# Kernel optimization log

Hardware: AMD Instinct MI355X
Metric: run time of the kernel (lower is better)

Reference implementation:

```python
import jax, jax.numpy as jnp
import numpy as np

BS, P, MAX_GT, C_IN, NCLS = 16, 4096, 32, 512, 4


def _make_boxes(key, shape):
    k1, k2, k3, k4 = jax.random.split(key, 4)
    x0 = jax.random.uniform(k1, shape) * 500.0
    y0 = jax.random.uniform(k2, shape) * 500.0
    w = 10.0 + jax.random.uniform(k3, shape) * 90.0
    h = 10.0 + jax.random.uniform(k4, shape) * 90.0
    return jnp.stack([x0, y0, x0 + w, y0 + h], -1)


def setup_inputs() -> dict:
    key = jax.random.key(0)
    ks = jax.random.split(key, 10)
    v = jax.random.normal(ks[0], (BS * P, C_IN), jnp.float32)
    rois = _make_boxes(ks[1], (BS, P))
    gt_boxes = _make_boxes(ks[2], (BS, MAX_GT))
    gt_counts = jax.random.randint(ks[3], (BS,), 0, MAX_GT + 1, jnp.int32)
    lab_idx = jax.random.randint(ks[4], (BS,), 0, NCLS)
    labels = jax.nn.one_hot(lab_idx, NCLS, dtype=jnp.float32)
    pre_score = jax.random.uniform(ks[5], (BS, P, NCLS), dtype=jnp.float32)
    cls_w = jax.random.normal(ks[6], (NCLS, C_IN), jnp.float32) * 0.01
    cls_b = jnp.full((NCLS,), -np.log((1.0 - 0.01) / 0.01), jnp.float32)
    reg_w = jax.random.normal(ks[7], (NCLS, C_IN), jnp.float32) * 0.01
    reg_b = jnp.zeros((NCLS,), jnp.float32)
    return {"v": v, "gt_boxes": gt_boxes, "gt_counts": gt_counts, "rois": rois,
            "labels": labels, "pre_score": pre_score, "cls_w": cls_w,
            "cls_b": cls_b, "reg_w": reg_w, "reg_b": reg_b}


def _box_iou(a, b):
    # a: (bs, Na, 4), b: (bs, Nb, 4) -> (bs, Na, Nb)
    area_a = (a[..., 2] - a[..., 0]) * (a[..., 3] - a[..., 1])
    area_b = (b[..., 2] - b[..., 0]) * (b[..., 3] - b[..., 1])
    lt = jnp.maximum(a[..., :, None, :2], b[..., None, :, :2])
    rb = jnp.minimum(a[..., :, None, 2:], b[..., None, :, 2:])
    wh = jnp.clip(rb - lt, 0.0)
    inter = wh[..., 0] * wh[..., 1]
    return inter / (area_a[..., :, None] + area_b[..., None, :] - inter)


def _ce(logits, tgt3):
    # CrossEntropyLoss(reduction='none'): logsumexp - logit[target]
    return jax.nn.logsumexp(logits, -1) - jnp.take_along_axis(logits, tgt3, -1)[..., 0]


def _smooth_l1(x):
    ax = jnp.abs(x)
    return jnp.where(ax < 1.0, 0.5 * ax * ax, ax - 0.5)


def reference(v, gt_boxes, gt_counts, rois, labels, pre_score, cls_w, cls_b, reg_w, reg_b):
    bs, Pn = rois.shape[:2]
    classify = (v @ cls_w.T + cls_b).reshape(bs, Pn, NCLS)
    reg = (v @ reg_w.T + reg_b).reshape(bs, Pn, NCLS)
    label = jnp.argmax(labels, 1)                                  # (bs,)
    lbl3 = jnp.broadcast_to(label[:, None, None], (bs, Pn, 1))

    # background branch: CE on raw logits, mean over proposals
    ce_bg = _ce(classify, lbl3).mean(1)                            # (bs,)

    # foreground branch: CE on clamped logits weighted by pre_score
    c = jnp.clip(classify, 1e-7, 1.0 - 1e-7)
    ps = jnp.take_along_axis(pre_score, lbl3, 2)[..., 0]           # (bs, P)
    ce_fg = _ce(c, lbl3) * ps

    gt_valid = jnp.arange(MAX_GT)[None, :] < gt_counts[:, None]    # (bs, MAX_GT)
    ious = _box_iou(gt_boxes, rois)                                # (bs, MAX_GT, P)
    ious = jnp.where(gt_valid[:, :, None], ious, -1.0)
    mask = jnp.any(ious > 0.5, 1).astype(classify.dtype)           # (bs, P)
    c_fg = (ce_fg * mask).sum(1) / (mask.sum(1) + 1e-7)

    idx = jnp.argmax(ious, 1)                                      # (bs, P)
    g = jnp.take_along_axis(gt_boxes, jnp.broadcast_to(idx[:, :, None], (bs, Pn, 4)), 1)
    gx = (g[..., 2] + g[..., 0]) / 2; gy = (g[..., 3] + g[..., 1]) / 2
    gw = (g[..., 2] - g[..., 0]) / 2; gh = (g[..., 3] - g[..., 1]) / 2
    r = rois
    rx = (r[..., 2] + r[..., 0]) / 2; ry = (r[..., 3] + r[..., 1]) / 2
    rw = (r[..., 2] - r[..., 0]) / 2; rh = (r[..., 3] - r[..., 1]) / 2
    tx = (gx - rx) / (rw + 1e-8); ty = (gy - ry) / (rh + 1e-8)
    tw = jnp.log(gw / (rw + 1e-8)); th = jnp.log(gh / (rh + 1e-8))
    t = jnp.stack([tx, ty, tw, th], -1)                            # (bs, P, 4)
    l1 = (_smooth_l1(reg - t).sum(-1) * mask * ps).sum(1) / (bs * Pn)

    has_gt = gt_counts > 0
    c_list = jnp.where(has_gt, c_fg, 0.0).sum()
    c_bg = jnp.where(has_gt, 0.0, ce_bg).sum()
    bg = jnp.where(has_gt, 0.0, float(Pn)).sum()
    l1_list = jnp.where(has_gt, l1, 0.0).sum()
    return (c_list + c_bg / (bg + 1e-7)) / (bs + 1e-7) + l1_list
```

## Files before the change

### kernel.cpp

```cpp
#include <hip/hip_runtime.h>
#include <math.h>

#define BSZ 16
#define NP 4096
#define MAXGT 32
#define CIN 512
#define NCLS 4
#define RPT 2
#define PB (64 * RPT)
#define NBLK (BSZ * NP / PB)
#define BPB (NP / PB)

__global__ __launch_bounds__(256, 2) void oicr_main(
    const float* __restrict__ v,
    const float* __restrict__ gt_boxes,
    const int*   __restrict__ gt_counts,
    const float* __restrict__ rois,
    const float* __restrict__ labels,
    const float* __restrict__ pre_score,
    const float* __restrict__ cls_w,
    const float* __restrict__ cls_b,
    const float* __restrict__ reg_w,
    const float* __restrict__ reg_b,
    float* __restrict__ partials)
{
    __shared__ float red8[4][PB][9];
    __shared__ float s_bias[8];
    __shared__ float g_x0[MAXGT], g_y0[MAXGT], g_x1[MAXGT], g_y1[MAXGT];
    __shared__ float g_area[MAXGT];
    __shared__ int   g_valid[MAXGT];
    __shared__ int   s_label;

    const int tid   = threadIdx.x;
    const int lane  = tid & 63;
    const int wv    = tid >> 6;
    const int b     = blockIdx.x >> 5;
    const int pbase = (blockIdx.x & 31) * PB;
    const int row0  = b * NP + pbase + lane;
    const int row1  = row0 + 64;

    if (tid < 8) s_bias[tid] = (tid < 4) ? cls_b[tid] : reg_b[tid - 4];
    if (tid < MAXGT) {
        int cnt = gt_counts[b];
        const float* g = gt_boxes + (size_t)(b * MAXGT + tid) * 4;
        float x0 = g[0], y0 = g[1], x1 = g[2], y1 = g[3];
        g_x0[tid] = x0; g_y0[tid] = y0; g_x1[tid] = x1; g_y1[tid] = y1;
        g_area[tid] = (x1 - x0) * (y1 - y0);
        g_valid[tid] = (tid < cnt) ? 1 : 0;
    }
    if (tid == 0) {
        const float* L = labels + b * NCLS;
        int bi = 0; float bv = L[0];
        #pragma unroll
        for (int c = 1; c < NCLS; ++c) { if (L[c] > bv) { bv = L[c]; bi = c; } }
        s_label = bi;
    }

    const int kq = __builtin_amdgcn_readfirstlane(wv);
    float acc0[8], acc1[8];
    #pragma unroll
    for (int c = 0; c < 8; ++c) { acc0[c] = 0.f; acc1[c] = 0.f; }

    const float4* vr0 = (const float4*)(v + (size_t)row0 * CIN) + kq * 32;
    const float4* vr1 = (const float4*)(v + (size_t)row1 * CIN) + kq * 32;

    #pragma unroll 8
    for (int i = 0; i < 32; ++i) {
        float4 a0 = vr0[i];
        float4 a1 = vr1[i];
        const int k = (kq * 32 + i) * 4;
        #pragma unroll
        for (int c = 0; c < 4; ++c) {
            float4 wc = *(const float4*)&cls_w[c * CIN + k];
            float4 wr = *(const float4*)&reg_w[c * CIN + k];
            acc0[c]     += a0.x * wc.x + a0.y * wc.y + a0.z * wc.z + a0.w * wc.w;
            acc1[c]     += a1.x * wc.x + a1.y * wc.y + a1.z * wc.z + a1.w * wc.w;
            acc0[4 + c] += a0.x * wr.x + a0.y * wr.y + a0.z * wr.z + a0.w * wr.w;
            acc1[4 + c] += a1.x * wr.x + a1.y * wr.y + a1.z * wr.z + a1.w * wr.w;
        }
    }

    #pragma unroll
    for (int c = 0; c < 8; ++c) {
        red8[wv][lane][c]      = acc0[c];
        red8[wv][64 + lane][c] = acc1[c];
    }
    __syncthreads();

    if (wv != 0) return;

    float px = 0.f, py = 0.f, pz = 0.f, pw = 0.f;

    #pragma unroll
    for (int rr = 0; rr < RPT; ++rr) {
        const int li  = rr * 64 + lane;
        const int row = row0 + rr * 64;

        float acc[8];
        #pragma unroll
        for (int c = 0; c < 8; ++c)
            acc[c] = red8[0][li][c] + red8[1][li][c] +
                     red8[2][li][c] + red8[3][li][c];

        const float cls0 = acc[0] + s_bias[0];
        const float cls1 = acc[1] + s_bias[1];
        const float cls2 = acc[2] + s_bias[2];
        const float cls3 = acc[3] + s_bias[3];
        const float reg0 = acc[4] + s_bias[4];
        const float reg1 = acc[5] + s_bias[5];
        const float reg2 = acc[6] + s_bias[6];
        const float reg3 = acc[7] + s_bias[7];

        const int lbl = s_label;

        float mB = fmaxf(fmaxf(cls0, cls1), fmaxf(cls2, cls3));
        float lseB = mB + logf(expf(cls0 - mB) + expf(cls1 - mB) +
                               expf(cls2 - mB) + expf(cls3 - mB));
        float clsL = (lbl == 0) ? cls0 : (lbl == 1) ? cls1 : (lbl == 2) ? cls2 : cls3;
        float ce_bg = lseB - clsL;

        const float lo = 1e-7f, hi = 1.f - 1e-7f;
        float cc0 = fminf(fmaxf(cls0, lo), hi);
        float cc1 = fminf(fmaxf(cls1, lo), hi);
        float cc2 = fminf(fmaxf(cls2, lo), hi);
        float cc3 = fminf(fmaxf(cls3, lo), hi);
        float mF = fmaxf(fmaxf(cc0, cc1), fmaxf(cc2, cc3));
        float lseF = mF + logf(expf(cc0 - mF) + expf(cc1 - mF) +
                               expf(cc2 - mF) + expf(cc3 - mF));
        float ccL = (lbl == 0) ? cc0 : (lbl == 1) ? cc1 : (lbl == 2) ? cc2 : cc3;
        float ce_fg = lseF - ccL;
        float ps = pre_score[(size_t)row * NCLS + lbl];

        float4 r = *(const float4*)(rois + (size_t)row * 4);
        float rarea = (r.z - r.x) * (r.w - r.y);
        float best = -3.0e38f;
        int   bi = 0;
        int   mk = 0;
        #pragma unroll
        for (int g = 0; g < MAXGT; ++g) {
            float ix0 = fmaxf(r.x, g_x0[g]);
            float iy0 = fmaxf(r.y, g_y0[g]);
            float ix1 = fminf(r.z, g_x1[g]);
            float iy1 = fminf(r.w, g_y1[g]);
            float iw = fmaxf(ix1 - ix0, 0.f);
            float ih = fmaxf(iy1 - iy0, 0.f);
            float inter = iw * ih;
            float iou = inter / (g_area[g] + rarea - inter);
            iou = g_valid[g] ? iou : -1.0f;
            if (iou > best) { best = iou; bi = g; }
            mk |= (iou > 0.5f) ? 1 : 0;
        }
        float maskf = mk ? 1.f : 0.f;

        float gx0 = g_x0[bi], gy0 = g_y0[bi], gx1 = g_x1[bi], gy1 = g_y1[bi];
        float gx = (gx1 + gx0) * 0.5f, gy = (gy1 + gy0) * 0.5f;
        float gw = (gx1 - gx0) * 0.5f, gh = (gy1 - gy0) * 0.5f;
        float rx = (r.z + r.x) * 0.5f, ry = (r.w + r.y) * 0.5f;
        float rw = (r.z - r.x) * 0.5f, rh = (r.w - r.y) * 0.5f;
        float tx = (gx - rx) / (rw + 1e-8f);
        float ty = (gy - ry) / (rh + 1e-8f);
        float tw = logf(gw / (rw + 1e-8f));
        float th = logf(gh / (rh + 1e-8f));

        float d0 = reg0 - tx, d1 = reg1 - ty, d2 = reg2 - tw, d3 = reg3 - th;
        float a0 = fabsf(d0), a1 = fabsf(d1), a2 = fabsf(d2), a3 = fabsf(d3);
        float s0 = (a0 < 1.f) ? 0.5f * a0 * a0 : a0 - 0.5f;
        float s1 = (a1 < 1.f) ? 0.5f * a1 * a1 : a1 - 0.5f;
        float s2 = (a2 < 1.f) ? 0.5f * a2 * a2 : a2 - 0.5f;
        float s3 = (a3 < 1.f) ? 0.5f * a3 * a3 : a3 - 0.5f;
        float sl1 = s0 + s1 + s2 + s3;

        px += ce_bg;
        py += ce_fg * ps * maskf;
        pz += maskf;
        pw += sl1 * maskf * ps;
    }

    #pragma unroll
    for (int off = 32; off > 0; off >>= 1) {
        px += __shfl_down(px, off);
        py += __shfl_down(py, off);
        pz += __shfl_down(pz, off);
        pw += __shfl_down(pw, off);
    }
    if (lane == 0) {
        partials[(size_t)blockIdx.x * 4 + 0] = px;
        partials[(size_t)blockIdx.x * 4 + 1] = py;
        partials[(size_t)blockIdx.x * 4 + 2] = pz;
        partials[(size_t)blockIdx.x * 4 + 3] = pw;
    }
}

__global__ __launch_bounds__(64) void oicr_final(
    const float* __restrict__ partials,
    const int*   __restrict__ gt_counts,
    float* __restrict__ out)
{
    const int lane = threadIdx.x;
    float S0 = 0.f, S1 = 0.f, S2 = 0.f, S3 = 0.f;
    float c_term = 0.f, cbg_term = 0.f, bg_term = 0.f, l1_term = 0.f;
    if (lane < BSZ) {
        for (int blk = 0; blk < BPB; ++blk) {
            const float* q = partials + (size_t)(lane * BPB + blk) * 4;
            S0 += q[0]; S1 += q[1]; S2 += q[2]; S3 += q[3];
        }
        bool has = gt_counts[lane] > 0;
        float c_fg       = S1 / (S2 + 1e-7f);
        float ce_bg_mean = S0 / (float)NP;
        float l1b        = S3 / (float)(BSZ * NP);
        c_term   = has ? c_fg : 0.f;
        cbg_term = has ? 0.f : ce_bg_mean;
        bg_term  = has ? 0.f : (float)NP;
        l1_term  = has ? l1b : 0.f;
    }
    #pragma unroll
    for (int off = 32; off > 0; off >>= 1) {
        c_term   += __shfl_down(c_term, off);
        cbg_term += __shfl_down(cbg_term, off);
        bg_term  += __shfl_down(bg_term, off);
        l1_term  += __shfl_down(l1_term, off);
    }
    if (lane == 0) {
        out[0] = (c_term + cbg_term / (bg_term + 1e-7f)) / ((float)BSZ + 1e-7f)
                 + l1_term;
    }
}

extern "C" void kernel_launch(void* const* d_in, const int* in_sizes, int n_in,
                              void* d_out, int out_size, void* d_ws, size_t ws_size,
                              hipStream_t stream)
{
    const float* v         = (const float*)d_in[0];
    const float* gt_boxes  = (const float*)d_in[1];
    const int*   gt_counts = (const int*)  d_in[2];
    const float* rois      = (const float*)d_in[3];
    const float* labels    = (const float*)d_in[4];
    const float* pre_score = (const float*)d_in[5];
    const float* cls_w     = (const float*)d_in[6];
    const float* cls_b     = (const float*)d_in[7];
    const float* reg_w     = (const float*)d_in[8];
    const float* reg_b     = (const float*)d_in[9];
    float* out      = (float*)d_out;
    float* partials = (float*)d_ws;

    oicr_main<<<dim3(NBLK), dim3(256), 0, stream>>>(
        v, gt_boxes, gt_counts, rois, labels, pre_score,
        cls_w, cls_b, reg_w, reg_b, partials);
    oicr_final<<<dim3(1), dim3(64), 0, stream>>>(partials, gt_counts, out);
}
```

Before: 42.68 us.

## Fuse final reduction into main kernel via last-block atomic counter

Removes the separate finalisation kernel. Each block publishes its partials and increments an atomic counter, and the last block to arrive performs the global reduction and writes the output. Loads of v become nontemporal loads. It adds a hipMemsetAsync per call to reset the counter, so a kernel launch is traded for a memset plus atomics.

```diff
diff --git a/kernel.cpp b/kernel.cpp
--- a/kernel.cpp
+++ b/kernel.cpp
@@ -11,7 +11,9 @@
 #define NBLK (BSZ * NP / PB)
 #define BPB (NP / PB)
 
-__global__ __launch_bounds__(256, 2) void oicr_main(
+typedef float f32x4 __attribute__((ext_vector_type(4)));
+
+__global__ __launch_bounds__(256, 2) void oicr_fused(
     const float* __restrict__ v,
     const float* __restrict__ gt_boxes,
     const int*   __restrict__ gt_counts,
@@ -22,7 +24,9 @@
     const float* __restrict__ cls_b,
     const float* __restrict__ reg_w,
     const float* __restrict__ reg_b,
-    float* __restrict__ partials)
+    float* __restrict__ partials,
+    unsigned int* __restrict__ counter,
+    float* __restrict__ out)
 {
     __shared__ float red8[4][PB][9];
     __shared__ float s_bias[8];
@@ -34,8 +38,9 @@
     const int tid   = threadIdx.x;
     const int lane  = tid & 63;
     const int wv    = tid >> 6;
-    const int b     = blockIdx.x >> 5;
-    const int pbase = (blockIdx.x & 31) * PB;
+    const int blk   = blockIdx.x;
+    const int b     = blk >> 5;
+    const int pbase = (blk & 31) * PB;
     const int row0  = b * NP + pbase + lane;
     const int row1  = row0 + 64;
 
@@ -61,22 +66,22 @@
     #pragma unroll
     for (int c = 0; c < 8; ++c) { acc0[c] = 0.f; acc1[c] = 0.f; }
 
-    const float4* vr0 = (const float4*)(v + (size_t)row0 * CIN) + kq * 32;
-    const float4* vr1 = (const float4*)(v + (size_t)row1 * CIN) + kq * 32;
+    const f32x4* vr0 = (const f32x4*)(v + (size_t)row0 * CIN) + kq * 32;
+    const f32x4* vr1 = (const f32x4*)(v + (size_t)row1 * CIN) + kq * 32;
 
     #pragma unroll 8
     for (int i = 0; i < 32; ++i) {
-        float4 a0 = vr0[i];
-        float4 a1 = vr1[i];
+        f32x4 a0 = __builtin_nontemporal_load(&vr0[i]);
+        f32x4 a1 = __builtin_nontemporal_load(&vr1[i]);
         const int k = (kq * 32 + i) * 4;
         #pragma unroll
         for (int c = 0; c < 4; ++c) {
-            float4 wc = *(const float4*)&cls_w[c * CIN + k];
-            float4 wr = *(const float4*)&reg_w[c * CIN + k];
-            acc0[c]     += a0.x * wc.x + a0.y * wc.y + a0.z * wc.z + a0.w * wc.w;
-            acc1[c]     += a1.x * wc.x + a1.y * wc.y + a1.z * wc.z + a1.w * wc.w;
-            acc0[4 + c] += a0.x * wr.x + a0.y * wr.y + a0.z * wr.z + a0.w * wr.w;
-            acc1[4 + c] += a1.x * wr.x + a1.y * wr.y + a1.z * wr.z + a1.w * wr.w;
+            const f32x4 wc = *(const f32x4*)&cls_w[c * CIN + k];
+            const f32x4 wr = *(const f32x4*)&reg_w[c * CIN + k];
+            acc0[c]     += a0[0]*wc[0] + a0[1]*wc[1] + a0[2]*wc[2] + a0[3]*wc[3];
+            acc1[c]     += a1[0]*wc[0] + a1[1]*wc[1] + a1[2]*wc[2] + a1[3]*wc[3];
+            acc0[4 + c] += a0[0]*wr[0] + a0[1]*wr[1] + a0[2]*wr[2] + a0[3]*wr[3];
+            acc1[4 + c] += a1[0]*wr[0] + a1[1]*wr[1] + a1[2]*wr[2] + a1[3]*wr[3];
         }
     }
 
@@ -119,11 +124,11 @@
         float clsL = (lbl == 0) ? cls0 : (lbl == 1) ? cls1 : (lbl == 2) ? cls2 : cls3;
         float ce_bg = lseB - clsL;
 
-        const float lo = 1e-7f, hi = 1.f - 1e-7f;
-        float cc0 = fminf(fmaxf(cls0, lo), hi);
-        float cc1 = fminf(fmaxf(cls1, lo), hi);
-        float cc2 = fminf(fmaxf(cls2, lo), hi);
-        float cc3 = fminf(fmaxf(cls3, lo), hi);
+        const float lo = 1e-7f, hi2 = 1.f - 1e-7f;
+        float cc0 = fminf(fmaxf(cls0, lo), hi2);
+        float cc1 = fminf(fmaxf(cls1, lo), hi2);
+        float cc2 = fminf(fmaxf(cls2, lo), hi2);
+        float cc3 = fminf(fmaxf(cls3, lo), hi2);
         float mF = fmaxf(fmaxf(cc0, cc1), fmaxf(cc2, cc3));
         float lseF = mF + logf(expf(cc0 - mF) + expf(cc1 - mF) +
                                expf(cc2 - mF) + expf(cc3 - mF));
@@ -183,46 +188,50 @@
         pz += __shfl_down(pz, off);
         pw += __shfl_down(pw, off);
     }
+
+    unsigned int old = 0;
     if (lane == 0) {
-        partials[(size_t)blockIdx.x * 4 + 0] = px;
-        partials[(size_t)blockIdx.x * 4 + 1] = py;
-        partials[(size_t)blockIdx.x * 4 + 2] = pz;
-        partials[(size_t)blockIdx.x * 4 + 3] = pw;
-    }
-}
-
-__global__ __launch_bounds__(64) void oicr_final(
-    const float* __restrict__ partials,
-    const int*   __restrict__ gt_counts,
-    float* __restrict__ out)
-{
-    const int lane = threadIdx.x;
-    float S0 = 0.f, S1 = 0.f, S2 = 0.f, S3 = 0.f;
-    float c_term = 0.f, cbg_term = 0.f, bg_term = 0.f, l1_term = 0.f;
-    if (lane < BSZ) {
-        for (int blk = 0; blk < BPB; ++blk) {
-            const float* q = partials + (size_t)(lane * BPB + blk) * 4;
-            S0 += q[0]; S1 += q[1]; S2 += q[2]; S3 += q[3];
-        }
-        bool has = gt_counts[lane] > 0;
-        float c_fg       = S1 / (S2 + 1e-7f);
-        float ce_bg_mean = S0 / (float)NP;
-        float l1b        = S3 / (float)(BSZ * NP);
-        c_term   = has ? c_fg : 0.f;
-        cbg_term = has ? 0.f : ce_bg_mean;
-        bg_term  = has ? 0.f : (float)NP;
-        l1_term  = has ? l1b : 0.f;
-    }
-    #pragma unroll
-    for (int off = 32; off > 0; off >>= 1) {
-        c_term   += __shfl_down(c_term, off);
-        cbg_term += __shfl_down(cbg_term, off);
-        bg_term  += __shfl_down(bg_term, off);
-        l1_term  += __shfl_down(l1_term, off);
-    }
-    if (lane == 0) {
-        out[0] = (c_term + cbg_term / (bg_term + 1e-7f)) / ((float)BSZ + 1e-7f)
-                 + l1_term;
+        float* q = partials + (size_t)blk * 4;
+        __hip_atomic_store(q + 0, px, __ATOMIC_RELAXED, __HIP_MEMORY_SCOPE_AGENT);
+        __hip_atomic_store(q + 1, py, __ATOMIC_RELAXED, __HIP_MEMORY_SCOPE_AGENT);
+        __hip_atomic_store(q + 2, pz, __ATOMIC_RELAXED, __HIP_MEMORY_SCOPE_AGENT);
+        __hip_atomic_store(q + 3, pw, __ATOMIC_RELAXED, __HIP_MEMORY_SCOPE_AGENT);
+        old = __hip_atomic_fetch_add(counter, 1u, __ATOMIC_ACQ_REL,
+                                     __HIP_MEMORY_SCOPE_AGENT);
+    }
+    old = (unsigned int)__shfl((int)old, 0, 64);
+    if (old == NBLK - 1) {
+        __threadfence();
+        float S0 = 0.f, S1 = 0.f, S2 = 0.f, S3 = 0.f;
+        float c_term = 0.f, cbg_term = 0.f, bg_term = 0.f, l1_term = 0.f;
+        if (lane < BSZ) {
+            for (int k = 0; k < BPB; ++k) {
+                float* q = partials + (size_t)(lane * BPB + k) * 4;
+                S0 += __hip_atomic_load(q + 0, __ATOMIC_RELAXED, __HIP_MEMORY_SCOPE_AGENT);
+                S1 += __hip_atomic_load(q + 1, __ATOMIC_RELAXED, __HIP_MEMORY_SCOPE_AGENT);
+                S2 += __hip_atomic_load(q + 2, __ATOMIC_RELAXED, __HIP_MEMORY_SCOPE_AGENT);
+                S3 += __hip_atomic_load(q + 3, __ATOMIC_RELAXED, __HIP_MEMORY_SCOPE_AGENT);
+            }
+            bool has = gt_counts[lane] > 0;
+            float c_fg       = S1 / (S2 + 1e-7f);
+            float ce_bg_mean = S0 / (float)NP;
+            float l1b        = S3 / (float)(BSZ * NP);
+            c_term   = has ? c_fg : 0.f;
+            cbg_term = has ? 0.f : ce_bg_mean;
+            bg_term  = has ? 0.f : (float)NP;
+            l1_term  = has ? l1b : 0.f;
+        }
+        #pragma unroll
+        for (int off = 32; off > 0; off >>= 1) {
+            c_term   += __shfl_down(c_term, off);
+            cbg_term += __shfl_down(cbg_term, off);
+            bg_term  += __shfl_down(bg_term, off);
+            l1_term  += __shfl_down(l1_term, off);
+        }
+        if (lane == 0) {
+            out[0] = (c_term + cbg_term / (bg_term + 1e-7f)) / ((float)BSZ + 1e-7f)
+                     + l1_term;
+        }
     }
 }
 
@@ -240,11 +249,13 @@
     const float* cls_b     = (const float*)d_in[7];
     const float* reg_w     = (const float*)d_in[8];
     const float* reg_b     = (const float*)d_in[9];
-    float* out      = (float*)d_out;
-    float* partials = (float*)d_ws;
-
-    oicr_main<<<dim3(NBLK), dim3(256), 0, stream>>>(
+    float* out = (float*)d_out;
+
+    unsigned int* counter = (unsigned int*)d_ws;
+    float* partials = (float*)((char*)d_ws + 256);
+
+    hipMemsetAsync(counter, 0, sizeof(unsigned int), stream);
+    oicr_fused<<<dim3(NBLK), dim3(256), 0, stream>>>(
         v, gt_boxes, gt_counts, rois, labels, pre_score,
-        cls_w, cls_b, reg_w, reg_b, partials);
-    oicr_final<<<dim3(1), dim3(64), 0, stream>>>(partials, gt_counts, out);
+        cls_w, cls_b, reg_w, reg_b, partials, counter, out);
 }
```

After: 98.68 us. 131% more time.
